# Kernel optimization log

Measured on AMD Instinct MI355X. Metric: run time of the kernel, lower is better.

Reference implementation:

```python
import jax, jax.numpy as jnp
import numpy as np

H = 2048   # hidden_size
NH = 16    # num_heads
D = 128    # head_dim_qk == head_dim_v
K = 4      # conv_kernel_size


def _causal_depthwise_conv(x, w, b):
    # x: [B,S,C], w: [C,K], b: [C]. Matches torch Conv1d(groups=C, padding=K-1)[..., :S]
    S = x.shape[1]
    xp = jnp.pad(x, ((0, 0), (K - 1, 0), (0, 0)))
    y = b
    for j in range(K):
        y = y + xp[:, j:j + S, :] * w[:, j]
    return y


def setup_inputs() -> dict:
    key = jax.random.key(0)
    ks = jax.random.split(key, 18)
    s = 0.02
    B, S = 2, 2048
    return {
        "x": jax.random.normal(ks[0], (B, S, H), dtype=jnp.float32),
        "Wq": jax.random.normal(ks[1], (H, NH * D), dtype=jnp.float32) * s,
        "Wk": jax.random.normal(ks[2], (H, NH * D), dtype=jnp.float32) * s,
        "Wv": jax.random.normal(ks[3], (H, NH * D), dtype=jnp.float32) * s,
        "Wa": jax.random.normal(ks[4], (H, NH), dtype=jnp.float32) * s,
        "ba": jax.random.normal(ks[5], (NH,), dtype=jnp.float32) * s,
        "Wb": jax.random.normal(ks[6], (H, NH), dtype=jnp.float32) * s,
        "bb": jax.random.normal(ks[7], (NH,), dtype=jnp.float32) * s,
        "Wg": jax.random.normal(ks[8], (H, NH * D), dtype=jnp.float32) * s,
        "Wo": jax.random.normal(ks[9], (NH * D, H), dtype=jnp.float32) * s,
        "qcw": jax.random.normal(ks[10], (NH * D, K), dtype=jnp.float32) * s,
        "qcb": jax.random.normal(ks[11], (NH * D,), dtype=jnp.float32) * s,
        "kcw": jax.random.normal(ks[12], (NH * D, K), dtype=jnp.float32) * s,
        "kcb": jax.random.normal(ks[13], (NH * D,), dtype=jnp.float32) * s,
        "vcw": jax.random.normal(ks[14], (NH * D, K), dtype=jnp.float32) * s,
        "vcb": jax.random.normal(ks[15], (NH * D,), dtype=jnp.float32) * s,
        "ln_w": jnp.ones((D,), dtype=jnp.float32),
        "ln_b": jnp.zeros((D,), dtype=jnp.float32),
    }


def _forward(x, Wq, Wk, Wv, Wa, ba, Wb, bb, Wg, Wo,
             qcw, qcb, kcw, kcb, vcw, vcb, ln_w, ln_b):
    B, S, _ = x.shape
    q = _causal_depthwise_conv(x @ Wq, qcw, qcb)
    k = _causal_depthwise_conv(x @ Wk, kcw, kcb)
    v = _causal_depthwise_conv(x @ Wv, vcw, vcb)
    q = jax.nn.silu(q).reshape(B, S, NH, D)
    k = jax.nn.silu(k).reshape(B, S, NH, D) * (D ** -0.5)
    v = jax.nn.silu(v).reshape(B, S, NH, D)
    alpha = jax.nn.sigmoid(x @ Wa + ba)  # [B,S,NH]
    beta = jax.nn.sigmoid(x @ Wb + bb)   # [B,S,NH]

    # time-major for scan
    qt = jnp.moveaxis(q, 1, 0)       # [S,B,NH,D]
    kt = jnp.moveaxis(k, 1, 0)
    vt = jnp.moveaxis(v, 1, 0)
    at = jnp.moveaxis(alpha, 1, 0)   # [S,B,NH]
    bt = jnp.moveaxis(beta, 1, 0)

    def step(St, inp):
        q_, k_, v_, a_, b_ = inp
        sk = jnp.einsum('bhij,bhj->bhi', St, k_)            # [B,NH,D]
        err = sk - v_
        Sn = (a_[..., None, None] * St
              - b_[..., None, None] * err[..., None] * k_[..., None, :])
        o_ = jnp.einsum('bhij,bhj->bhi', Sn, q_)
        return Sn, o_

    S0 = jnp.zeros((B, NH, D, D), dtype=x.dtype)
    _, o = jax.lax.scan(step, S0, (qt, kt, vt, at, bt))
    o = jnp.moveaxis(o, 0, 1)  # [B,S,NH,D]

    # LayerNorm over head_dim
    mu = jnp.mean(o, axis=-1, keepdims=True)
    var = jnp.mean(jnp.square(o - mu), axis=-1, keepdims=True)
    o = (o - mu) * jax.lax.rsqrt(var + 1e-5) * ln_w + ln_b

    g = jax.nn.sigmoid(x @ Wg).reshape(B, S, NH, D)
    o = (o * g).reshape(B, S, NH * D)
    return o @ Wo


def reference(x, Wq, Wk, Wv, Wa, ba, Wb, bb, Wg, Wo,
              qcw, qcb, kcw, kcb, vcw, vcb, ln_w, ln_b):
    return _forward(x, Wq, Wk, Wv, Wa, ba, Wb, bb, Wg, Wo,
                    qcw, qcb, kcw, kcb, vcw, vcb, ln_w, ln_b)
```

## Files before the change

kernel.cpp:

```cpp
#include <hip/hip_runtime.h>
#include <math.h>
#include <stdint.h>

typedef unsigned short u16;
typedef unsigned int u32;
typedef __attribute__((ext_vector_type(8))) short short8;
typedef __attribute__((ext_vector_type(4))) float f32x4;

#define MFMA16(a, b, c) __builtin_amdgcn_mfma_f32_16x16x32_bf16(a, b, c, 0, 0, 0)

__device__ __forceinline__ u16 f2bf(float f) {
  union { float f; u32 u; } v; v.f = f;
  return (u16)((v.u + 0x7FFFu + ((v.u >> 16) & 1u)) >> 16);
}
__device__ __forceinline__ float bf2f(u16 h) {
  union { u32 u; float f; } v; v.u = ((u32)h) << 16; return v.f;
}
__device__ __forceinline__ float bflo(u32 p) {
  union { u32 u; float f; } v; v.u = p << 16; return v.f;
}
__device__ __forceinline__ float bfhi(u32 p) {
  union { u32 u; float f; } v; v.u = p & 0xffff0000u; return v.f;
}
__device__ __forceinline__ float sigm(float x) { return 1.f / (1.f + expf(-x)); }

__global__ void k_cvt_x(const float* __restrict__ x, u16* __restrict__ xb) {
  int i = (blockIdx.x * 256 + threadIdx.x) * 8;
  float4 a = *(const float4*)(x + i);
  float4 b = *(const float4*)(x + i + 4);
  uint4 p;
  p.x = (u32)f2bf(a.x) | ((u32)f2bf(a.y) << 16);
  p.y = (u32)f2bf(a.z) | ((u32)f2bf(a.w) << 16);
  p.z = (u32)f2bf(b.x) | ((u32)f2bf(b.y) << 16);
  p.w = (u32)f2bf(b.z) | ((u32)f2bf(b.w) << 16);
  *(uint4*)(xb + i) = p;
}

__global__ void k_tconv4(const float* __restrict__ W0, const float* __restrict__ W1,
                         const float* __restrict__ W2, const float* __restrict__ W3,
                         u16* __restrict__ Wt) {
  __shared__ float tile[32][33];
  int z = blockIdx.z;
  const float* W = (z == 0) ? W0 : (z == 1) ? W1 : (z == 2) ? W2 : W3;
  u16* dst = Wt + (size_t)z * 2048 * 2048;
  int n0 = blockIdx.x * 32, k0 = blockIdx.y * 32;
  int tc = threadIdx.x & 31, tr = threadIdx.x >> 5;
  #pragma unroll
  for (int p = 0; p < 4; ++p) {
    int k = k0 + p * 8 + tr;
    tile[p * 8 + tr][tc] = W[(size_t)k * 2048 + n0 + tc];
  }
  __syncthreads();
  #pragma unroll
  for (int p = 0; p < 4; ++p) {
    int n = n0 + p * 8 + tr;
    dst[(size_t)n * 2048 + k0 + tc] = f2bf(tile[tc][p * 8 + tr]);
  }
}

__global__ void k_tconv(const float* __restrict__ W, u16* __restrict__ Wt) {
  __shared__ float tile[32][33];
  int n0 = blockIdx.x * 32, k0 = blockIdx.y * 32;
  int tc = threadIdx.x & 31, tr = threadIdx.x >> 5;
  #pragma unroll
  for (int p = 0; p < 4; ++p) {
    int k = k0 + p * 8 + tr;
    tile[p * 8 + tr][tc] = W[(size_t)k * 2048 + n0 + tc];
  }
  __syncthreads();
  #pragma unroll
  for (int p = 0; p < 4; ++p) {
    int n = n0 + p * 8 + tr;
    Wt[(size_t)n * 2048 + k0 + tc] = f2bf(tile[tc][p * 8 + tr]);
  }
}

__global__ __launch_bounds__(256)
void k_ab(const float* __restrict__ x, const float* __restrict__ Wa,
          const float* __restrict__ ba, const float* __restrict__ Wb,
          const float* __restrict__ bb, float* __restrict__ ab2) {
  __shared__ float Wl[128 * 32];
  __shared__ float xl[8][128];
  const int t = threadIdx.x;
  const int lr = t >> 5, c = t & 31;
  const int r0 = blockIdx.x * 8;
  const int ch = c & 15;
  float acc = 0.f;
  for (int kt = 0; kt < 16; ++kt) {
    #pragma unroll
    for (int i = 0; i < 16; ++i) {
      int idx = i * 256 + t;
      int kk = idx >> 5, cc = idx & 31;
      const float* Ws = (cc < 16) ? Wa : Wb;
      Wl[kk * 32 + cc] = Ws[(kt * 128 + kk) * 16 + (cc & 15)];
    }
    #pragma unroll
    for (int i = 0; i < 4; ++i) {
      int idx = i * 256 + t;
      int rr = idx >> 7, kk = idx & 127;
      xl[rr][kk] = x[(size_t)(r0 + rr) * 2048 + kt * 128 + kk];
    }
    __syncthreads();
    #pragma unroll
    for (int kk = 0; kk < 128; kk += 4) {
      float2 x01 = *(const float2*)&xl[lr][kk];
      float2 x23 = *(const float2*)&xl[lr][kk + 2];
      acc += x01.x * Wl[(kk + 0) * 32 + c] + x01.y * Wl[(kk + 1) * 32 + c]
           + x23.x * Wl[(kk + 2) * 32 + c] + x23.y * Wl[(kk + 3) * 32 + c];
    }
    __syncthreads();
  }
  acc += (c < 16) ? ba[ch] : bb[ch];
  float sg = sigm(acc);
  int rowi = r0 + lr;
  int b = rowi >> 11, s = rowi & 2047;
  size_t base = ((size_t)(b * 16 + ch) * 2048 + s) * 2;
  if (c < 16) ab2[base + 0] = sg;
  else        ab2[base + 1] = sg;
}

__device__ __forceinline__ void gld_lds16(const u16* g, u16* l) {
  __builtin_amdgcn_global_load_lds((const __attribute__((address_space(1))) void*)g,
                                   (__attribute__((address_space(3))) void*)l, 16, 0, 0);
}

template <int MODE>
__global__ void k_gemm(const u16* __restrict__ A, const u16* __restrict__ Bw,
                       void* C0, void* C1, int Kd) {
  __shared__ u16 As[2][128 * 32];
  __shared__ u16 Bs[2][128 * 32];
  const int t = threadIdx.x;
  const int lane = t & 63, wv = t >> 6;
  const int wr = wv >> 1, wc = wv & 1;
  const int m0 = blockIdx.y * 128, n0 = blockIdx.x * 128;
  f32x4 acc[4][4] = {};
  const int NT = Kd / 32;

  auto stage = [&](int buf, int kt) {
    #pragma unroll
    for (int i = 0; i < 2; ++i) {
      int li = i * 256 + t;
      int row = li >> 2, kc = li & 3;
      int kcs = kc ^ ((row >> 1) & 3);
      const u16* ga = A + (size_t)(m0 + row) * Kd + kt * 32 + kcs * 8;
      gld_lds16(ga, &As[buf][(i * 256 + wv * 64) * 8]);
      const u16* gb = Bw + (size_t)(n0 + row) * Kd + kt * 32 + kcs * 8;
      gld_lds16(gb, &Bs[buf][(i * 256 + wv * 64) * 8]);
    }
  };

  stage(0, 0);
  __syncthreads();
  int buf = 0;
  const int l15 = lane & 15, l4 = lane >> 4;
  for (int kt = 0; kt < NT; ++kt) {
    if (kt + 1 < NT) stage(buf ^ 1, kt + 1);
    short8 af[4], bfr[4];
    #pragma unroll
    for (int m = 0; m < 4; ++m) {
      int row = wr * 64 + m * 16 + l15;
      int g = l4 ^ ((row >> 1) & 3);
      af[m] = *(const short8*)&As[buf][row * 32 + g * 8];
    }
    #pragma unroll
    for (int n = 0; n < 4; ++n) {
      int row = wc * 64 + n * 16 + l15;
      int g = l4 ^ ((row >> 1) & 3);
      bfr[n] = *(const short8*)&Bs[buf][row * 32 + g * 8];
    }
    #pragma unroll
    for (int m = 0; m < 4; ++m)
      #pragma unroll
      for (int n = 0; n < 4; ++n)
        acc[m][n] = MFMA16(af[m], bfr[n], acc[m][n]);
    __syncthreads();
    buf ^= 1;
  }
  #pragma unroll
  for (int m = 0; m < 4; ++m)
    #pragma unroll
    for (int n = 0; n < 4; ++n)
      #pragma unroll
      for (int e = 0; e < 4; ++e) {
        int row = m0 + wr * 64 + m * 16 + l4 * 4 + e;
        int col = n0 + wc * 64 + n * 16 + l15;
        if (MODE == 0) {
          ((float*)C0)[(size_t)row * 2048 + col] = acc[m][n][e];
        } else {
          u16 vb = f2bf(acc[m][n][e]);
          if (n0 < 6144) ((u16*)C0)[(size_t)row * 6144 + col] = vb;
          else           ((u16*)C1)[(size_t)row * 2048 + (col - 6144)] = vb;
        }
      }
}

template <int MODE>
__global__ __launch_bounds__(512)
void k_gemm8(const u16* __restrict__ A, const u16* __restrict__ Bw,
             void* C0, void* C1) {
  __shared__ u16 lds[65536];
  const int t = threadIdx.x;
  const int w = t >> 6, lane = t & 63;
  const int l15 = lane & 15, l4 = lane >> 4;
  const int wm = w >> 2, wn = w & 3;
  const int bid = blockIdx.x;
  const int mt = ((bid & 7) << 1) | ((bid >> 3) & 1);
  const int nt = bid >> 4;
  const int m0 = mt * 256, n0 = nt * 256;

  f32x4 acc[8][4] = {};
  short8 a[4][2], b[4][2];

  auto stageHalf = [&](int buf, int kt, int mat, int half) {
    const u16* src = mat ? Bw : A;
    const int row0 = (mat ? n0 : m0) + half * 128;
    u16* dst0 = &lds[mat * 32768 + (buf * 2 + half) * 8192 + w * 1024];
    #pragma unroll
    for (int i = 0; i < 2; ++i) {
      int f = w * 128 + i * 64 + lane;
      int rr = f >> 3, g = f & 7;
      const u16* ga = src + (size_t)(row0 + rr) * 2048 + kt * 64 + ((g ^ (rr & 7)) << 3);
      gld_lds16(ga, dst0 + i * 512);
    }
  };
  auto rdA = [&](int buf, int mq, int ks) {
    int row = wm * 64 + (mq & 3) * 16 + l15;
    int g = (l4 + ks * 4) ^ (row & 7);
    return *(const short8*)&lds[(buf * 2 + (mq >> 2)) * 8192 + row * 64 + g * 8];
  };
  auto rdB = [&](int buf, int n, int ks) {
    int row = wn * 32 + (n & 1) * 16 + l15;
    int g = (l4 + ks * 4) ^ (row & 7);
    return *(const short8*)&lds[32768 + (buf * 2 + (n >> 1)) * 8192 + row * 64 + g * 8];
  };

  stageHalf(0, 0, 0, 0); stageHalf(0, 0, 1, 0);
  stageHalf(0, 0, 1, 1); stageHalf(0, 0, 0, 1);
  asm volatile("s_waitcnt vmcnt(0)" ::: "memory");
  __builtin_amdgcn_s_barrier();
  __builtin_amdgcn_sched_barrier(0);

  for (int kt = 0; kt < 32; ++kt) {
    const int bufc = kt & 1, bufn = bufc ^ 1;
    const int ktn = (kt + 1 < 32) ? kt + 1 : 31;

    stageHalf(bufn, ktn, 0, 0);
    stageHalf(bufn, ktn, 1, 0);
    stageHalf(bufn, ktn, 1, 1);
    #pragma unroll
    for (int mq = 0; mq < 4; ++mq) { a[mq][0] = rdA(bufc, mq, 0); a[mq][1] = rdA(bufc, mq, 1); }
    #pragma unroll
    for (int n = 0; n < 4; ++n) { b[n][0] = rdB(bufc, n, 0); b[n][1] = rdB(bufc, n, 1); }
    __builtin_amdgcn_s_setprio(1);
    #pragma unroll
    for (int mq = 0; mq < 4; ++mq)
      #pragma unroll
      for (int n = 0; n < 4; ++n) {
        acc[mq][n] = MFMA16(a[mq][0], b[n][0], acc[mq][n]);
        acc[mq][n] = MFMA16(a[mq][1], b[n][1], acc[mq][n]);
      }
    __builtin_amdgcn_s_setprio(0);
    asm volatile("s_waitcnt vmcnt(6)" ::: "memory");
    __builtin_amdgcn_s_barrier();
    __builtin_amdgcn_sched_barrier(0);

    stageHalf(bufn, ktn, 0, 1);
    #pragma unroll
    for (int mq = 0; mq < 4; ++mq) { a[mq][0] = rdA(bufc, mq + 4, 0); a[mq][1] = rdA(bufc, mq + 4, 1); }
    __builtin_amdgcn_s_setprio(1);
    #pragma unroll
    for (int mq = 0; mq < 4; ++mq)
      #pragma unroll
      for (int n = 0; n < 4; ++n) {
        acc[mq + 4][n] = MFMA16(a[mq][0], b[n][0], acc[mq + 4][n]);
        acc[mq + 4][n] = MFMA16(a[mq][1], b[n][1], acc[mq + 4][n]);
      }
    __builtin_amdgcn_s_setprio(0);
    asm volatile("s_waitcnt vmcnt(2)" ::: "memory");
    __builtin_amdgcn_s_barrier();
    __builtin_amdgcn_sched_barrier(0);
  }

  const bool toG = (MODE == 1) && (n0 >= 6144);
  #pragma unroll
  for (int mq = 0; mq < 8; ++mq) {
    int row = m0 + (mq >> 2) * 128 + wm * 64 + (mq & 3) * 16 + l4 * 4;
    #pragma unroll
    for (int n = 0; n < 4; ++n) {
      int col = n0 + (n >> 1) * 128 + wn * 32 + (n & 1) * 16 + l15;
      #pragma unroll
      for (int e = 0; e < 4; ++e) {
        if (MODE == 0) {
          ((float*)C0)[(size_t)(row + e) * 2048 + col] = acc[mq][n][e];
        } else {
          u16 vb = f2bf(acc[mq][n][e]);
          if (!toG) ((u16*)C0)[(size_t)(row + e) * 6144 + col] = vb;
          else      ((u16*)C1)[(size_t)(row + e) * 2048 + (col - 6144)] = vb;
        }
      }
    }
  }
}

__global__ void k_conv(const u16* __restrict__ projQKV,
                       const float* __restrict__ qcw, const float* __restrict__ qcb,
                       const float* __restrict__ kcw, const float* __restrict__ kcb,
                       const float* __restrict__ vcw, const float* __restrict__ vcb,
                       u16* __restrict__ qkv2) {
  int idx = blockIdx.x * 256 + threadIdx.x;
  int cq = idx % 1536, rrow = idx / 1536;
  int c = cq * 4;
  int s = rrow & 2047, b = rrow >> 11;
  int type = c >> 11;
  int ch = c & 2047;
  int h = ch >> 7, d = ch & 127;
  const float* cw; const float* cb;
  if (type == 0)      { cw = qcw; cb = qcb; }
  else if (type == 1) { cw = kcw; cb = kcb; }
  else                { cw = vcw; cb = vcb; }
  float wch[4][4];
  #pragma unroll
  for (int u = 0; u < 4; ++u) {
    float4 wv = *(const float4*)(cw + (ch + u) * 4);
    wch[u][0] = wv.x; wch[u][1] = wv.y; wch[u][2] = wv.z; wch[u][3] = wv.w;
  }
  float4 bv = *(const float4*)(cb + ch);
  float accv[4] = {bv.x, bv.y, bv.z, bv.w};
  #pragma unroll
  for (int j = 0; j < 4; ++j) {
    int sj = s - 3 + j;
    if (sj < 0) continue;
    const u16* p = projQKV + (size_t)(rrow + j - 3) * 6144 + c;
    u32 pa = *(const u32*)p;
    u32 pb = *(const u32*)(p + 2);
    accv[0] += bflo(pa) * wch[0][j];
    accv[1] += bfhi(pa) * wch[1][j];
    accv[2] += bflo(pb) * wch[2][j];
    accv[3] += bfhi(pb) * wch[3][j];
  }
  u16 o4[4];
  #pragma unroll
  for (int u = 0; u < 4; ++u) {
    float y = accv[u];
    float sv = y * sigm(y);
    if (type == 1) sv *= 0.08838834764831845f;
    o4[u] = f2bf(sv);
  }
  int off = (type == 1 ? 0 : (type == 0 ? 128 : 256)) + d;
  u16* dst = qkv2 + ((size_t)(b * 16 + h) * 2048 + s) * 384 + off;
  *(u32*)dst       = (u32)o4[0] | ((u32)o4[1] << 16);
  *(u32*)(dst + 2) = (u32)o4[2] | ((u32)o4[3] << 16);
}

__global__ __launch_bounds__(256)
void k_chunkA(const u16* __restrict__ qkv2, const float* __restrict__ ab2,
              u16* __restrict__ Tbv, u16* __restrict__ nTbk,
              u16* __restrict__ Aq, float* __restrict__ vecs,
              u16* __restrict__ Kt) {
  __shared__ u16 Kl[64][136], Ql[64][136];
  __shared__ float Gk[4096], Gq[4096];
  __shared__ float clL[64], laL[64], bL[64], gpL[64];
  const int unit = blockIdx.x;
  const int bh = unit >> 5, c = unit & 31;
  const int t = threadIdx.x;
  const int wv = t >> 6, lane = t & 63;
  const int l15 = lane & 15, l4 = lane >> 4;
  const u16* qb = qkv2 + ((size_t)bh * 2048 + c * 64) * 384;

  #pragma unroll
  for (int p = 0; p < 4; ++p) {
    int ld = p * 256 + t;
    int row = ld >> 4, c8 = (ld & 15) * 8;
    *(uint4*)&Kl[row][c8] = *(const uint4*)(qb + (size_t)row * 384 + c8);
    *(uint4*)&Ql[row][c8] = *(const uint4*)(qb + (size_t)row * 384 + 128 + c8);
  }
  if (wv == 0) {
    float2 abv = *(const float2*)(ab2 + ((size_t)bh * 2048 + c * 64 + lane) * 2);
    float la = log2f(abv.x);
    float cl = la;
    #pragma unroll
    for (int o = 1; o < 64; o <<= 1) {
      float nv = __shfl_up(cl, o, 64);
      if (lane >= o) cl += nv;
    }
    clL[lane] = cl; laL[lane] = la; bL[lane] = abv.y;
    gpL[lane] = exp2f(cl - la);
  }
  __syncthreads();

  {
    const int t0 = (wv >> 1) * 32, i0 = (wv & 1) * 32;
    f32x4 ak[2][2] = {}, aq[2][2] = {};
    #pragma unroll
    for (int ks = 0; ks < 4; ++ks) {
      short8 bk[2], Ka[2], Qa[2];
      #pragma unroll
      for (int n = 0; n < 2; ++n)
        bk[n] = *(const short8*)&Kl[i0 + n * 16 + l15][ks * 32 + l4 * 8];
      #pragma unroll
      for (int m = 0; m < 2; ++m) {
        Ka[m] = *(const short8*)&Kl[t0 + m * 16 + l15][ks * 32 + l4 * 8];
        Qa[m] = *(const short8*)&Ql[t0 + m * 16 + l15][ks * 32 + l4 * 8];
      }
      #pragma unroll
      for (int m = 0; m < 2; ++m)
        #pragma unroll
        for (int n = 0; n < 2; ++n) {
          ak[m][n] = MFMA16(Ka[m], bk[n], ak[m][n]);
          aq[m][n] = MFMA16(Qa[m], bk[n], aq[m][n]);
        }
    }
    #pragma unroll
    for (int m = 0; m < 2; ++m)
      #pragma unroll
      for (int n = 0; n < 2; ++n)
        #pragma unroll
        for (int e = 0; e < 4; ++e) {
          int row = t0 + m * 16 + l4 * 4 + e;
          int col = i0 + n * 16 + l15;
          Gk[row * 64 + col] = ak[m][n][e];
          Gq[row * 64 + col] = aq[m][n][e];
        }
  }
  __syncthreads();

  #pragma unroll
  for (int p = 0; p < 16; ++p) {
    int e = p * 256 + t; int tt = e >> 6, ii = e & 63;
    float lv = 0.f;
    if (ii < tt) lv = bL[tt] * Gk[e] * exp2f(clL[tt] - laL[tt] - clL[ii]);
    float av = (ii <= tt) ? Gq[e] * exp2f(clL[tt] - clL[ii]) : 0.f;
    Gk[e] = lv;
    Aq[(size_t)unit * 4096 + e] = f2bf(av);
  }
  __syncthreads();

  float X[64];
  if (t < 128) {
    #pragma unroll
    for (int r = 0; r < 64; ++r)
      X[r] = bL[r] * bf2f(qb[(size_t)r * 384 + 256 + t]);
  } else {
    int ck = t - 128;
    #pragma unroll
    for (int r = 0; r < 64; ++r)
      X[r] = -bL[r] * gpL[r] * bf2f(Kl[r][ck]);
  }
  #pragma unroll
  for (int i = 0; i < 63; ++i) {
    float xi = X[i];
    #pragma unroll
    for (int r = i + 1; r < 64; ++r)
      X[r] = fmaf(-Gk[r * 64 + i], xi, X[r]);
  }
  if (t < 128) {
    #pragma unroll
    for (int r = 0; r < 64; ++r)
      Tbv[(size_t)unit * 8192 + r * 128 + t] = f2bf(X[r]);
  } else {
    #pragma unroll
    for (int r = 0; r < 64; ++r)
      nTbk[(size_t)unit * 8192 + r * 128 + (t - 128)] = f2bf(X[r]);
  }
  if (t < 64) {
    vecs[(size_t)unit * 128 + t] = exp2f(clL[t]);
    vecs[(size_t)unit * 128 + 64 + t] = exp2f(clL[63] - clL[t]);
  }
  {
    int dk = t >> 1, tt0 = (t & 1) * 32;
    uint4 w[4];
    u16* wp = (u16*)w;
    #pragma unroll
    for (int j = 0; j < 32; ++j) wp[j] = Kl[tt0 + j][dk];
    uint4* dst = (uint4*)(Kt + (size_t)unit * 8192 + dk * 64 + tt0);
    dst[0] = w[0]; dst[1] = w[1]; dst[2] = w[2]; dst[3] = w[3];
  }
}

#define OFF_NT  0
#define OFF_AQ  8192
#define OFF_Q   12288
#define OFF_KT  20480
#define OFF_TBV 28672
#define STG_U16 29696

__global__ __launch_bounds__(256)
void k_chunkB(const u16* __restrict__ qkv2, const u16* __restrict__ Tbv,
              const u16* __restrict__ nTbk, const u16* __restrict__ Aq,
              const u16* __restrict__ Kt, const float* __restrict__ vecs,
              float* __restrict__ o) {
  __shared__ u16 stg[2][STG_U16];
  __shared__ float S[16 * 132];
  __shared__ u16 Ut[16 * 72], Utd[16 * 72];
  __shared__ float gdl[2][128];
  const int bid = blockIdx.x;
  const int xcd = bid & 7, within = bid >> 3;
  const int sl = within & 7, hgrp = within >> 3;
  const int bh = hgrp * 8 + xcd;
  const int dv0 = sl * 16;
  const int b = bh >> 4, h = bh & 15;
  const int t = threadIdx.x;
  const int wv = t >> 6, lane = t & 63;
  const int l15 = lane & 15, l4 = lane >> 4;
  const int t0 = wv * 16;
  const int dk0 = wv * 32;
  const u16* qbase = qkv2 + (size_t)bh * 2048 * 384;
  float* obase = o + (size_t)b * 2048 * 2048 + h * 128 + dv0;

  for (int p = t; p < 16 * 132; p += 256) S[p] = 0.f;

  auto stage = [&](int buf, int c) {
    u16* sb = &stg[buf][0];
    const size_t unit = (size_t)bh * 32 + c;
    const u16* tbk = nTbk + unit * 8192;
    const u16* aqp = Aq + unit * 4096;
    const u16* ktp = Kt + unit * 8192;
    const u16* tbv = Tbv + unit * 8192;
    const u16* qp  = qbase + (size_t)c * 64 * 384 + 128;
    #pragma unroll
    for (int r = 0; r < 4; ++r) {
      int f = r * 256 + t; int rr = f >> 4, c16 = f & 15;
      gld_lds16(tbk + rr * 128 + (c16 ^ (rr & 7)) * 8, sb + OFF_NT + (r * 256 + wv * 64) * 8);
    }
    #pragma unroll
    for (int r = 0; r < 2; ++r) {
      int f = r * 256 + t; int rr = f >> 3, c8 = f & 7;
      gld_lds16(aqp + rr * 64 + (c8 ^ (rr & 7)) * 8, sb + OFF_AQ + (r * 256 + wv * 64) * 8);
    }
    #pragma unroll
    for (int r = 0; r < 4; ++r) {
      int f = r * 256 + t; int rr = f >> 4, c16 = f & 15;
      gld_lds16(qp + rr * 384 + (c16 ^ (rr & 7)) * 8, sb + OFF_Q + (r * 256 + wv * 64) * 8);
    }
    #pragma unroll
    for (int r = 0; r < 4; ++r) {
      int f = r * 256 + t; int rr = f >> 3, c8 = f & 7;
      gld_lds16(ktp + rr * 64 + (c8 ^ (rr & 7)) * 8, sb + OFF_KT + (r * 256 + wv * 64) * 8);
    }
    if (t < 128)
      gld_lds16(tbv + (t >> 1) * 128 + dv0 + (t & 1) * 8, sb + OFF_TBV + wv * 64 * 8);
  };

  stage(0, 0);
  if (t < 128) gdl[0][t] = vecs[(size_t)bh * 32 * 128 + t];
  __syncthreads();

  for (int c = 0; c < 32; ++c) {
    const int buf = c & 1;
    const u16* sb = &stg[buf][0];
    float vnext = 0.f;
    if (c + 1 < 32) {
      stage(buf ^ 1, c + 1);
      if (t < 128) vnext = vecs[((size_t)bh * 32 + c + 1) * 128 + t];
    }

    f32x4 acc1 = {}, acc2 = {};
    #pragma unroll
    for (int e = 0; e < 4; ++e)
      acc1[e] = bf2f(sb[OFF_TBV + (t0 + l4 * 4 + e) * 16 + l15]);
    #pragma unroll
    for (int ks = 0; ks < 4; ++ks) {
      short8 bhi, blo;
      {
        const float* srow = &S[l15 * 132 + ks * 32 + l4 * 8];
        float4 s0 = *(const float4*)srow, s1 = *(const float4*)(srow + 4);
        float sv[8] = {s0.x, s0.y, s0.z, s0.w, s1.x, s1.y, s1.z, s1.w};
        #pragma unroll
        for (int j = 0; j < 8; ++j) {
          u16 hv = f2bf(sv[j]);
          bhi[j] = (short)hv;
          blo[j] = (short)f2bf(sv[j] - bf2f(hv));
        }
      }
      const int cx = ((ks * 4 + l4) ^ (l15 & 7)) * 8;
      short8 a1 = *(const short8*)&sb[OFF_NT + (t0 + l15) * 128 + cx];
      short8 a2 = *(const short8*)&sb[OFF_Q + (t0 + l15) * 128 + cx];
      acc1 = MFMA16(a1, bhi, acc1);
      acc1 = MFMA16(a1, blo, acc1);
      acc2 = MFMA16(a2, bhi, acc2);
      acc2 = MFMA16(a2, blo, acc2);
    }
    {
      u16 up[4], ud[4];
      #pragma unroll
      for (int e = 0; e < 4; ++e) {
        float uv = acc1[e];
        up[e] = f2bf(uv);
        ud[e] = f2bf(uv * gdl[buf][64 + t0 + l4 * 4 + e]);
      }
      int ux = l15 * 72 + t0 + l4 * 4;
      *(u32*)&Ut[ux]      = (u32)up[0] | ((u32)up[1] << 16);
      *(u32*)&Ut[ux + 2]  = (u32)up[2] | ((u32)up[3] << 16);
      *(u32*)&Utd[ux]     = (u32)ud[0] | ((u32)ud[1] << 16);
      *(u32*)&Utd[ux + 2] = (u32)ud[2] | ((u32)ud[3] << 16);
    }
    asm volatile("s_waitcnt lgkmcnt(0)" ::: "memory");
    __builtin_amdgcn_s_barrier();
    __builtin_amdgcn_sched_barrier(0);

    #pragma unroll
    for (int e = 0; e < 4; ++e) acc2[e] *= gdl[buf][t0 + l4 * 4 + e];
    #pragma unroll
    for (int ks = 0; ks < 2; ++ks) {
      const int cx = ((ks * 4 + l4) ^ (l15 & 7)) * 8;
      short8 af = *(const short8*)&sb[OFF_AQ + (t0 + l15) * 64 + cx];
      short8 bf_ = *(const short8*)&Ut[l15 * 72 + ks * 32 + l4 * 8];
      acc2 = MFMA16(af, bf_, acc2);
    }
    #pragma unroll
    for (int e = 0; e < 4; ++e)
      obase[(size_t)(c * 64 + t0 + l4 * 4 + e) * 2048 + l15] = acc2[e];

    f32x4 acc3[2] = {};
    #pragma unroll
    for (int ks = 0; ks < 2; ++ks) {
      short8 a3 = *(const short8*)&Utd[l15 * 72 + ks * 32 + l4 * 8];
      #pragma unroll
      for (int n = 0; n < 2; ++n) {
        const int kr = dk0 + n * 16 + l15;
        const int cx = ((ks * 4 + l4) ^ (l15 & 7)) * 8;
        short8 b3 = *(const short8*)&sb[OFF_KT + kr * 64 + cx];
        acc3[n] = MFMA16(a3, b3, acc3[n]);
      }
    }
    float gtot = gdl[buf][63];
    #pragma unroll
    for (int n = 0; n < 2; ++n)
      #pragma unroll
      for (int e = 0; e < 4; ++e) {
        float* sp = &S[(l4 * 4 + e) * 132 + dk0 + n * 16 + l15];
        *sp = gtot * *sp + acc3[n][e];
      }
    if (c + 1 < 32 && t < 128) gdl[buf ^ 1][t] = vnext;
    __syncthreads();
  }
}

__global__ void k_lng(const float* __restrict__ o, const u16* __restrict__ projG,
                      const float* __restrict__ ln_w, const float* __restrict__ ln_b,
                      u16* __restrict__ og) {
  int gidx = blockIdx.x * 4 + (threadIdx.x >> 6);
  int lane = threadIdx.x & 63;
  int rrow = gidx >> 4, h = gidx & 15;
  const float* op = o + (size_t)rrow * 2048 + h * 128;
  float2 x2 = *(const float2*)(op + lane * 2);
  float sum = x2.x + x2.y, sq = x2.x * x2.x + x2.y * x2.y;
  #pragma unroll
  for (int m = 1; m < 64; m <<= 1) {
    sum += __shfl_xor(sum, m, 64);
    sq  += __shfl_xor(sq, m, 64);
  }
  float mu = sum * (1.f / 128.f);
  float var = sq * (1.f / 128.f) - mu * mu;
  float rs = 1.0f / sqrtf(var + 1e-5f);
  u32 gu = *(const u32*)(projG + (size_t)rrow * 2048 + h * 128 + lane * 2);
  float g0 = sigm(bflo(gu)), g1 = sigm(bfhi(gu));
  int d0 = lane * 2;
  float y0 = ((x2.x - mu) * rs * ln_w[d0] + ln_b[d0]) * g0;
  float y1 = ((x2.y - mu) * rs * ln_w[d0 + 1] + ln_b[d0 + 1]) * g1;
  *(u32*)(og + (size_t)rrow * 2048 + h * 128 + d0) = (u32)f2bf(y0) | ((u32)f2bf(y1) << 16);
}

extern "C" void kernel_launch(void* const* d_in, const int* in_sizes, int n_in,
                              void* d_out, int out_size, void* d_ws, size_t ws_size,
                              hipStream_t stream) {
  const float* x   = (const float*)d_in[0];
  const float* Wq  = (const float*)d_in[1];
  const float* Wk  = (const float*)d_in[2];
  const float* Wv  = (const float*)d_in[3];
  const float* Wa  = (const float*)d_in[4];
  const float* ba  = (const float*)d_in[5];
  const float* Wb  = (const float*)d_in[6];
  const float* bb  = (const float*)d_in[7];
  const float* Wg  = (const float*)d_in[8];
  const float* Wo  = (const float*)d_in[9];
  const float* qcw = (const float*)d_in[10];
  const float* qcb = (const float*)d_in[11];
  const float* kcw = (const float*)d_in[12];
  const float* kcb = (const float*)d_in[13];
  const float* vcw = (const float*)d_in[14];
  const float* vcb = (const float*)d_in[15];
  const float* lnw = (const float*)d_in[16];
  const float* lnb = (const float*)d_in[17];
  float* out = (float*)d_out;

  if (ws_size < 168820736ull) return;
  char* ws = (char*)d_ws;
  u16*   xb   = (u16*)(ws);
  u16*   Kt   = (u16*)(ws);
  u16*   og   = (u16*)(ws);
  u16*   Wt   = (u16*)(ws + 16777216);
  u16*   Wot  = (u16*)(ws + 16777216);
  u16*   Tbv  = (u16*)(ws + 25165824);
  u16*   Aq   = (u16*)(ws + 41943040);
  u16*   pQKV = (u16*)(ws + 50331648);
  float* oB   = (float*)(ws + 50331648);
  u16*   nTbk = (u16*)(ws + 83886080);
  u16*   pG   = (u16*)(ws + 100663296);
  u16*   qkv2 = (u16*)(ws + 117440512);
  float* ab2  = (float*)(ws + 167772160);
  float* vecs = (float*)(ws + 168296448);

  k_cvt_x<<<4096, 256, 0, stream>>>(x, xb);
  k_tconv4<<<dim3(64, 64, 4), 256, 0, stream>>>(Wq, Wk, Wv, Wg, Wt);
  k_ab<<<512, 256, 0, stream>>>(x, Wa, ba, Wb, bb, ab2);

  k_gemm8<1><<<512, 512, 0, stream>>>(xb, Wt, pQKV, pG);
  k_tconv<<<dim3(64, 64), 256, 0, stream>>>(Wo, Wot);
  k_conv<<<24576, 256, 0, stream>>>(pQKV, qcw, qcb, kcw, kcb, vcw, vcb, qkv2);
  k_chunkA<<<1024, 256, 0, stream>>>(qkv2, ab2, Tbv, nTbk, Aq, vecs, Kt);
  k_chunkB<<<256, 256, 0, stream>>>(qkv2, Tbv, nTbk, Aq, Kt, vecs, oB);
  k_lng<<<16384, 256, 0, stream>>>(oB, pG, lnw, lnb, og);
  k_gemm<0><<<dim3(16, 32), 256, 0, stream>>>(og, Wot, out, nullptr, 2048);
}
```

Before: 465.5 us.

## Restructure QKVG GEMM main loop into 8-phase ping-pong schedule with quarter-tile staging

Rewrites the k_gemm8 main loop to process two k-tiles per iteration in eight phases. Each phase interleaves LDS fragment reads, one half-tile global-to-LDS stage, and a quarter of the MFMA block, separated by barriers, with both buffers preloaded before the loop. The aim is finer overlap of global loads, LDS reads and matrix math across waves. The block mapping also changes from a swizzled 1D grid to a plain 2D grid, which gives up the L2-friendly tile ordering and adds many more barriers per k-tile.

```diff
diff --git a/kernel.cpp b/kernel.cpp
--- a/kernel.cpp
+++ b/kernel.cpp
@@ -194,6 +194,10 @@
       }
 }
 
+#define SBAR __builtin_amdgcn_s_barrier()
+#define SCHB __builtin_amdgcn_sched_barrier(0)
+#define LGKM0 asm volatile("s_waitcnt lgkmcnt(0)" ::: "memory")
+
 template <int MODE>
 __global__ __launch_bounds__(512)
 void k_gemm8(const u16* __restrict__ A, const u16* __restrict__ Bw,
@@ -203,10 +207,7 @@
   const int w = t >> 6, lane = t & 63;
   const int l15 = lane & 15, l4 = lane >> 4;
   const int wm = w >> 2, wn = w & 3;
-  const int bid = blockIdx.x;
-  const int mt = ((bid & 7) << 1) | ((bid >> 3) & 1);
-  const int nt = bid >> 4;
-  const int m0 = mt * 256, n0 = nt * 256;
+  const int m0 = blockIdx.y * 256, n0 = blockIdx.x * 256;
 
   f32x4 acc[8][4] = {};
   short8 a[4][2], b[4][2];
@@ -233,52 +234,83 @@
     int g = (l4 + ks * 4) ^ (row & 7);
     return *(const short8*)&lds[32768 + (buf * 2 + (n >> 1)) * 8192 + row * 64 + g * 8];
   };
-
-  stageHalf(0, 0, 0, 0); stageHalf(0, 0, 1, 0);
-  stageHalf(0, 0, 1, 1); stageHalf(0, 0, 0, 1);
+  auto quad = [&](int mB, int nB) {
+    #pragma unroll
+    for (int mq = 0; mq < 4; ++mq)
+      #pragma unroll
+      for (int nn = 0; nn < 2; ++nn) {
+        acc[mB + mq][nB + nn] = MFMA16(a[mq][0], b[nB + nn][0], acc[mB + mq][nB + nn]);
+        acc[mB + mq][nB + nn] = MFMA16(a[mq][1], b[nB + nn][1], acc[mB + mq][nB + nn]);
+      }
+  };
+
+  stageHalf(0, 0, 0, 0); stageHalf(0, 0, 1, 0); stageHalf(0, 0, 1, 1); stageHalf(0, 0, 0, 1);
+  stageHalf(1, 1, 0, 0); stageHalf(1, 1, 1, 0); stageHalf(1, 1, 1, 1); stageHalf(1, 1, 0, 1);
   asm volatile("s_waitcnt vmcnt(0)" ::: "memory");
-  __builtin_amdgcn_s_barrier();
-  __builtin_amdgcn_sched_barrier(0);
-
-  for (int kt = 0; kt < 32; ++kt) {
-    const int bufc = kt & 1, bufn = bufc ^ 1;
-    const int ktn = (kt + 1 < 32) ? kt + 1 : 31;
-
-    stageHalf(bufn, ktn, 0, 0);
-    stageHalf(bufn, ktn, 1, 0);
-    stageHalf(bufn, ktn, 1, 1);
-    #pragma unroll
-    for (int mq = 0; mq < 4; ++mq) { a[mq][0] = rdA(bufc, mq, 0); a[mq][1] = rdA(bufc, mq, 1); }
-    #pragma unroll
-    for (int n = 0; n < 4; ++n) { b[n][0] = rdB(bufc, n, 0); b[n][1] = rdB(bufc, n, 1); }
-    __builtin_amdgcn_s_setprio(1);
-    #pragma unroll
-    for (int mq = 0; mq < 4; ++mq)
-      #pragma unroll
-      for (int n = 0; n < 4; ++n) {
-        acc[mq][n] = MFMA16(a[mq][0], b[n][0], acc[mq][n]);
-        acc[mq][n] = MFMA16(a[mq][1], b[n][1], acc[mq][n]);
-      }
-    __builtin_amdgcn_s_setprio(0);
+  SBAR; SCHB;
+
+  for (int it = 0; it < 16; ++it) {
+    const int kt0 = 2 * it;
+    const int st0 = (it < 15) ? kt0 + 2 : kt0;
+    const int st1 = (it < 15) ? kt0 + 3 : kt0 + 1;
+
+    #pragma unroll
+    for (int mq = 0; mq < 4; ++mq) { a[mq][0] = rdA(0, mq, 0); a[mq][1] = rdA(0, mq, 1); }
+    #pragma unroll
+    for (int n = 0; n < 2; ++n) { b[n][0] = rdB(0, n, 0); b[n][1] = rdB(0, n, 1); }
+    SCHB; SBAR; LGKM0; SCHB;
+    __builtin_amdgcn_s_setprio(1); quad(0, 0); __builtin_amdgcn_s_setprio(0);
+    SBAR; SCHB;
+
+    #pragma unroll
+    for (int n = 2; n < 4; ++n) { b[n][0] = rdB(0, n, 0); b[n][1] = rdB(0, n, 1); }
+    stageHalf(0, st0, 0, 0);
+    SCHB; SBAR; LGKM0; SCHB;
+    __builtin_amdgcn_s_setprio(1); quad(0, 2); __builtin_amdgcn_s_setprio(0);
+    SBAR; SCHB;
+
+    #pragma unroll
+    for (int mq = 0; mq < 4; ++mq) { a[mq][0] = rdA(0, mq + 4, 0); a[mq][1] = rdA(0, mq + 4, 1); }
+    stageHalf(0, st0, 1, 0);
+    SCHB; SBAR; LGKM0; SCHB;
+    __builtin_amdgcn_s_setprio(1); quad(4, 2); __builtin_amdgcn_s_setprio(0);
+    SBAR; SCHB;
+
+    stageHalf(0, st0, 1, 1);
+    SCHB; SBAR; LGKM0; SCHB;
+    __builtin_amdgcn_s_setprio(1); quad(4, 0); __builtin_amdgcn_s_setprio(0);
     asm volatile("s_waitcnt vmcnt(6)" ::: "memory");
-    __builtin_amdgcn_s_barrier();
-    __builtin_amdgcn_sched_barrier(0);
-
-    stageHalf(bufn, ktn, 0, 1);
-    #pragma unroll
-    for (int mq = 0; mq < 4; ++mq) { a[mq][0] = rdA(bufc, mq + 4, 0); a[mq][1] = rdA(bufc, mq + 4, 1); }
-    __builtin_amdgcn_s_setprio(1);
-    #pragma unroll
-    for (int mq = 0; mq < 4; ++mq)
-      #pragma unroll
-      for (int n = 0; n < 4; ++n) {
-        acc[mq + 4][n] = MFMA16(a[mq][0], b[n][0], acc[mq + 4][n]);
-        acc[mq + 4][n] = MFMA16(a[mq][1], b[n][1], acc[mq + 4][n]);
-      }
-    __builtin_amdgcn_s_setprio(0);
-    asm volatile("s_waitcnt vmcnt(2)" ::: "memory");
-    __builtin_amdgcn_s_barrier();
-    __builtin_amdgcn_sched_barrier(0);
+    SBAR; SCHB;
+
+    #pragma unroll
+    for (int mq = 0; mq < 4; ++mq) { a[mq][0] = rdA(1, mq, 0); a[mq][1] = rdA(1, mq, 1); }
+    #pragma unroll
+    for (int n = 0; n < 2; ++n) { b[n][0] = rdB(1, n, 0); b[n][1] = rdB(1, n, 1); }
+    stageHalf(0, st0, 0, 1);
+    SCHB; SBAR; LGKM0; SCHB;
+    __builtin_amdgcn_s_setprio(1); quad(0, 0); __builtin_amdgcn_s_setprio(0);
+    SBAR; SCHB;
+
+    #pragma unroll
+    for (int n = 2; n < 4; ++n) { b[n][0] = rdB(1, n, 0); b[n][1] = rdB(1, n, 1); }
+    stageHalf(1, st1, 0, 0);
+    SCHB; SBAR; LGKM0; SCHB;
+    __builtin_amdgcn_s_setprio(1); quad(0, 2); __builtin_amdgcn_s_setprio(0);
+    SBAR; SCHB;
+
+    #pragma unroll
+    for (int mq = 0; mq < 4; ++mq) { a[mq][0] = rdA(1, mq + 4, 0); a[mq][1] = rdA(1, mq + 4, 1); }
+    stageHalf(1, st1, 1, 0);
+    SCHB; SBAR; LGKM0; SCHB;
+    __builtin_amdgcn_s_setprio(1); quad(4, 2); __builtin_amdgcn_s_setprio(0);
+    SBAR; SCHB;
+
+    stageHalf(1, st1, 1, 1);
+    stageHalf(1, st1, 0, 1);
+    SCHB; SBAR; LGKM0; SCHB;
+    __builtin_amdgcn_s_setprio(1); quad(4, 0); __builtin_amdgcn_s_setprio(0);
+    asm volatile("s_waitcnt vmcnt(8)" ::: "memory");
+    SBAR; SCHB;
   }
 
   const bool toG = (MODE == 1) && (n0 >= 6144);
@@ -705,7 +737,7 @@
   k_tconv4<<<dim3(64, 64, 4), 256, 0, stream>>>(Wq, Wk, Wv, Wg, Wt);
   k_ab<<<512, 256, 0, stream>>>(x, Wa, ba, Wb, bb, ab2);
 
-  k_gemm8<1><<<512, 512, 0, stream>>>(xb, Wt, pQKV, pG);
+  k_gemm8<1><<<dim3(32, 16), 512, 0, stream>>>(xb, Wt, pQKV, pG);
   k_tconv<<<dim3(64, 64), 256, 0, stream>>>(Wo, Wot);
   k_conv<<<24576, 256, 0, stream>>>(pQKV, qcw, qcb, kcw, kcb, vcw, vcb, qkv2);
   k_chunkA<<<1024, 256, 0, stream>>>(qkv2, ab2, Tbv, nTbk, Aq, vecs, Kt);
```

Measured after the change: 471.7 us. About the same (+1.3%).

## Simplify QKVG GEMM to single-phase K=32 double-buffered loop with plain syncs

Applied to the files above, without the earlier changes.

Replaces the hand-scheduled two-phase K=64 pipeline in the fused QKV/gate GEMM with a simpler loop over K=32 tiles, halving LDS usage. It drops the staggered half-tile staging, vmcnt waits, priority hints and the swizzled block-to-tile mapping, switching to a 2D grid and __syncthreads. Less LDS may allow more occupancy, but it doubles barrier count and loses fine-grained overlap and L2-friendly tile ordering.

```diff
diff --git a/kernel.cpp b/kernel.cpp
--- a/kernel.cpp
+++ b/kernel.cpp
@@ -198,87 +198,55 @@
 __global__ __launch_bounds__(512)
 void k_gemm8(const u16* __restrict__ A, const u16* __restrict__ Bw,
              void* C0, void* C1) {
-  __shared__ u16 lds[65536];
+  __shared__ u16 lds[32768];
   const int t = threadIdx.x;
   const int w = t >> 6, lane = t & 63;
   const int l15 = lane & 15, l4 = lane >> 4;
   const int wm = w >> 2, wn = w & 3;
-  const int bid = blockIdx.x;
-  const int mt = ((bid & 7) << 1) | ((bid >> 3) & 1);
-  const int nt = bid >> 4;
-  const int m0 = mt * 256, n0 = nt * 256;
+  const int m0 = blockIdx.y * 256, n0 = blockIdx.x * 256;
 
   f32x4 acc[8][4] = {};
-  short8 a[4][2], b[4][2];
-
-  auto stageHalf = [&](int buf, int kt, int mat, int half) {
-    const u16* src = mat ? Bw : A;
-    const int row0 = (mat ? n0 : m0) + half * 128;
-    u16* dst0 = &lds[mat * 32768 + (buf * 2 + half) * 8192 + w * 1024];
+
+  auto stage = [&](int buf, int kt) {
     #pragma unroll
     for (int i = 0; i < 2; ++i) {
       int f = w * 128 + i * 64 + lane;
-      int rr = f >> 3, g = f & 7;
-      const u16* ga = src + (size_t)(row0 + rr) * 2048 + kt * 64 + ((g ^ (rr & 7)) << 3);
-      gld_lds16(ga, dst0 + i * 512);
+      int rr = f >> 2, g = f & 3;
+      int gs = g ^ ((rr >> 1) & 3);
+      const u16* ga = A + (size_t)(m0 + rr) * 2048 + kt * 32 + gs * 8;
+      gld_lds16(ga, &lds[buf * 8192 + f * 8]);
+      const u16* gb = Bw + (size_t)(n0 + rr) * 2048 + kt * 32 + gs * 8;
+      gld_lds16(gb, &lds[16384 + buf * 8192 + f * 8]);
     }
   };
-  auto rdA = [&](int buf, int mq, int ks) {
-    int row = wm * 64 + (mq & 3) * 16 + l15;
-    int g = (l4 + ks * 4) ^ (row & 7);
-    return *(const short8*)&lds[(buf * 2 + (mq >> 2)) * 8192 + row * 64 + g * 8];
+  auto rdA = [&](int buf, int mq) {
+    int row = (mq >> 2) * 128 + wm * 64 + (mq & 3) * 16 + l15;
+    int g = l4 ^ ((row >> 1) & 3);
+    return *(const short8*)&lds[buf * 8192 + row * 32 + g * 8];
   };
-  auto rdB = [&](int buf, int n, int ks) {
-    int row = wn * 32 + (n & 1) * 16 + l15;
-    int g = (l4 + ks * 4) ^ (row & 7);
-    return *(const short8*)&lds[32768 + (buf * 2 + (n >> 1)) * 8192 + row * 64 + g * 8];
+  auto rdB = [&](int buf, int n) {
+    int row = (n >> 1) * 128 + wn * 32 + (n & 1) * 16 + l15;
+    int g = l4 ^ ((row >> 1) & 3);
+    return *(const short8*)&lds[16384 + buf * 8192 + row * 32 + g * 8];
   };
 
-  stageHalf(0, 0, 0, 0); stageHalf(0, 0, 1, 0);
-  stageHalf(0, 0, 1, 1); stageHalf(0, 0, 0, 1);
-  asm volatile("s_waitcnt vmcnt(0)" ::: "memory");
-  __builtin_amdgcn_s_barrier();
-  __builtin_amdgcn_sched_barrier(0);
-
-  for (int kt = 0; kt < 32; ++kt) {
-    const int bufc = kt & 1, bufn = bufc ^ 1;
-    const int ktn = (kt + 1 < 32) ? kt + 1 : 31;
-
-    stageHalf(bufn, ktn, 0, 0);
-    stageHalf(bufn, ktn, 1, 0);
-    stageHalf(bufn, ktn, 1, 1);
-    #pragma unroll
-    for (int mq = 0; mq < 4; ++mq) { a[mq][0] = rdA(bufc, mq, 0); a[mq][1] = rdA(bufc, mq, 1); }
-    #pragma unroll
-    for (int n = 0; n < 4; ++n) { b[n][0] = rdB(bufc, n, 0); b[n][1] = rdB(bufc, n, 1); }
-    __builtin_amdgcn_s_setprio(1);
-    #pragma unroll
-    for (int mq = 0; mq < 4; ++mq)
-      #pragma unroll
-      for (int n = 0; n < 4; ++n) {
-        acc[mq][n] = MFMA16(a[mq][0], b[n][0], acc[mq][n]);
-        acc[mq][n] = MFMA16(a[mq][1], b[n][1], acc[mq][n]);
-      }
-    __builtin_amdgcn_s_setprio(0);
-    asm volatile("s_waitcnt vmcnt(6)" ::: "memory");
-    __builtin_amdgcn_s_barrier();
-    __builtin_amdgcn_sched_barrier(0);
-
-    stageHalf(bufn, ktn, 0, 1);
-    #pragma unroll
-    for (int mq = 0; mq < 4; ++mq) { a[mq][0] = rdA(bufc, mq + 4, 0); a[mq][1] = rdA(bufc, mq + 4, 1); }
-    __builtin_amdgcn_s_setprio(1);
-    #pragma unroll
-    for (int mq = 0; mq < 4; ++mq)
-      #pragma unroll
-      for (int n = 0; n < 4; ++n) {
-        acc[mq + 4][n] = MFMA16(a[mq][0], b[n][0], acc[mq + 4][n]);
-        acc[mq + 4][n] = MFMA16(a[mq][1], b[n][1], acc[mq + 4][n]);
-      }
-    __builtin_amdgcn_s_setprio(0);
-    asm volatile("s_waitcnt vmcnt(2)" ::: "memory");
-    __builtin_amdgcn_s_barrier();
-    __builtin_amdgcn_sched_barrier(0);
+  stage(0, 0);
+  __syncthreads();
+
+  for (int kt = 0; kt < 64; ++kt) {
+    const int buf = kt & 1;
+    if (kt + 1 < 64) stage(buf ^ 1, kt + 1);
+    short8 a[8], b[4];
+    #pragma unroll
+    for (int mq = 0; mq < 8; ++mq) a[mq] = rdA(buf, mq);
+    #pragma unroll
+    for (int n = 0; n < 4; ++n) b[n] = rdB(buf, n);
+    #pragma unroll
+    for (int mq = 0; mq < 8; ++mq)
+      #pragma unroll
+      for (int n = 0; n < 4; ++n)
+        acc[mq][n] = MFMA16(a[mq], b[n], acc[mq][n]);
+    __syncthreads();
   }
 
   const bool toG = (MODE == 1) && (n0 >= 6144);
@@ -705,7 +673,7 @@
   k_tconv4<<<dim3(64, 64, 4), 256, 0, stream>>>(Wq, Wk, Wv, Wg, Wt);
   k_ab<<<512, 256, 0, stream>>>(x, Wa, ba, Wb, bb, ab2);
 
-  k_gemm8<1><<<512, 512, 0, stream>>>(xb, Wt, pQKV, pG);
+  k_gemm8<1><<<dim3(32, 16), 512, 0, stream>>>(xb, Wt, pQKV, pG);
   k_tconv<<<dim3(64, 64), 256, 0, stream>>>(Wo, Wot);
   k_conv<<<24576, 256, 0, stream>>>(pQKV, qcw, qcb, kcw, kcb, vcw, vcb, qkv2);
   k_chunkA<<<1024, 256, 0, stream>>>(qkv2, ab2, Tbv, nTbk, Aq, vecs, Kt);
```

New measurement: 470.9 us. No clear change (+1.2%).

## Fuse causal conv and SiLU into chunkA, drop separate conv kernel

Applied to the files above, without the earlier changes.

Removes the standalone k_conv kernel and its qkv2 intermediate buffer. chunkA now computes the depthwise causal conv and SiLU for q, k and v directly from the projection output, and writes a compact Q buffer for chunkB. The gemm8 grid is also changed from a swizzled 1D block mapping to a plain 2D grid. This saves a full write and read of the qkv2 intermediate, at the cost of redundant halo row loads and more work inside chunkA. The gemm8 grid change may lose the cache locality the swizzle was providing.

```diff
diff --git a/kernel.cpp b/kernel.cpp
--- a/kernel.cpp
+++ b/kernel.cpp
@@ -203,10 +203,7 @@
   const int w = t >> 6, lane = t & 63;
   const int l15 = lane & 15, l4 = lane >> 4;
   const int wm = w >> 2, wn = w & 3;
-  const int bid = blockIdx.x;
-  const int mt = ((bid & 7) << 1) | ((bid >> 3) & 1);
-  const int nt = bid >> 4;
-  const int m0 = mt * 256, n0 = nt * 256;
+  const int m0 = blockIdx.y * 256, n0 = blockIdx.x * 256;
 
   f32x4 acc[8][4] = {};
   short8 a[4][2], b[4][2];
@@ -302,77 +299,79 @@
   }
 }
 
-__global__ void k_conv(const u16* __restrict__ projQKV,
-                       const float* __restrict__ qcw, const float* __restrict__ qcb,
-                       const float* __restrict__ kcw, const float* __restrict__ kcb,
-                       const float* __restrict__ vcw, const float* __restrict__ vcb,
-                       u16* __restrict__ qkv2) {
-  int idx = blockIdx.x * 256 + threadIdx.x;
-  int cq = idx % 1536, rrow = idx / 1536;
-  int c = cq * 4;
-  int s = rrow & 2047, b = rrow >> 11;
-  int type = c >> 11;
-  int ch = c & 2047;
-  int h = ch >> 7, d = ch & 127;
-  const float* cw; const float* cb;
-  if (type == 0)      { cw = qcw; cb = qcb; }
-  else if (type == 1) { cw = kcw; cb = kcb; }
-  else                { cw = vcw; cb = vcb; }
-  float wch[4][4];
-  #pragma unroll
-  for (int u = 0; u < 4; ++u) {
-    float4 wv = *(const float4*)(cw + (ch + u) * 4);
-    wch[u][0] = wv.x; wch[u][1] = wv.y; wch[u][2] = wv.z; wch[u][3] = wv.w;
-  }
-  float4 bv = *(const float4*)(cb + ch);
-  float accv[4] = {bv.x, bv.y, bv.z, bv.w};
-  #pragma unroll
-  for (int j = 0; j < 4; ++j) {
-    int sj = s - 3 + j;
-    if (sj < 0) continue;
-    const u16* p = projQKV + (size_t)(rrow + j - 3) * 6144 + c;
-    u32 pa = *(const u32*)p;
-    u32 pb = *(const u32*)(p + 2);
-    accv[0] += bflo(pa) * wch[0][j];
-    accv[1] += bfhi(pa) * wch[1][j];
-    accv[2] += bflo(pb) * wch[2][j];
-    accv[3] += bfhi(pb) * wch[3][j];
-  }
-  u16 o4[4];
-  #pragma unroll
-  for (int u = 0; u < 4; ++u) {
-    float y = accv[u];
-    float sv = y * sigm(y);
-    if (type == 1) sv *= 0.08838834764831845f;
-    o4[u] = f2bf(sv);
-  }
-  int off = (type == 1 ? 0 : (type == 0 ? 128 : 256)) + d;
-  u16* dst = qkv2 + ((size_t)(b * 16 + h) * 2048 + s) * 384 + off;
-  *(u32*)dst       = (u32)o4[0] | ((u32)o4[1] << 16);
-  *(u32*)(dst + 2) = (u32)o4[2] | ((u32)o4[3] << 16);
-}
-
 __global__ __launch_bounds__(256)
-void k_chunkA(const u16* __restrict__ qkv2, const float* __restrict__ ab2,
+void k_chunkA(const u16* __restrict__ proj, const float* __restrict__ ab2,
+              const float* __restrict__ qcw, const float* __restrict__ qcb,
+              const float* __restrict__ kcw, const float* __restrict__ kcb,
+              const float* __restrict__ vcw, const float* __restrict__ vcb,
               u16* __restrict__ Tbv, u16* __restrict__ nTbk,
               u16* __restrict__ Aq, float* __restrict__ vecs,
-              u16* __restrict__ Kt) {
+              u16* __restrict__ Kt, u16* __restrict__ Qd) {
   __shared__ u16 Kl[64][136], Ql[64][136];
   __shared__ float Gk[4096], Gq[4096];
   __shared__ float clL[64], laL[64], bL[64], gpL[64];
   const int unit = blockIdx.x;
   const int bh = unit >> 5, c = unit & 31;
+  const int b = bh >> 4, h = bh & 15;
+  const int s0 = c * 64;
   const int t = threadIdx.x;
   const int wv = t >> 6, lane = t & 63;
   const int l15 = lane & 15, l4 = lane >> 4;
-  const u16* qb = qkv2 + ((size_t)bh * 2048 + c * 64) * 384;
-
-  #pragma unroll
-  for (int p = 0; p < 4; ++p) {
-    int ld = p * 256 + t;
-    int row = ld >> 4, c8 = (ld & 15) * 8;
-    *(uint4*)&Kl[row][c8] = *(const uint4*)(qb + (size_t)row * 384 + c8);
-    *(uint4*)&Ql[row][c8] = *(const uint4*)(qb + (size_t)row * 384 + 128 + c8);
+  const u16* projb = proj + (size_t)b * 2048 * 6144;
+
+  {
+    const int tr = t >> 4, c8 = (t & 15) * 8;
+    const int ch0 = h * 128 + c8;
+    float4 wk[8], wq[8];
+    float bk[8], bq[8];
+    #pragma unroll
+    for (int u = 0; u < 8; ++u) {
+      wk[u] = *(const float4*)(kcw + (ch0 + u) * 4);
+      wq[u] = *(const float4*)(qcw + (ch0 + u) * 4);
+    }
+    {
+      float4 b0 = *(const float4*)(kcb + ch0); float4 b1 = *(const float4*)(kcb + ch0 + 4);
+      bk[0]=b0.x; bk[1]=b0.y; bk[2]=b0.z; bk[3]=b0.w; bk[4]=b1.x; bk[5]=b1.y; bk[6]=b1.z; bk[7]=b1.w;
+      float4 c0 = *(const float4*)(qcb + ch0); float4 c1 = *(const float4*)(qcb + ch0 + 4);
+      bq[0]=c0.x; bq[1]=c0.y; bq[2]=c0.z; bq[3]=c0.w; bq[4]=c1.x; bq[5]=c1.y; bq[6]=c1.z; bq[7]=c1.w;
+    }
+    #pragma unroll
+    for (int p = 0; p < 4; ++p) {
+      int row = p * 16 + tr;
+      int s = s0 + row;
+      float ak[8], aq_[8];
+      #pragma unroll
+      for (int u = 0; u < 8; ++u) { ak[u] = bk[u]; aq_[u] = bq[u]; }
+      #pragma unroll
+      for (int j = 0; j < 4; ++j) {
+        int sj = s - 3 + j;
+        if (sj < 0) continue;
+        const u16* rk = projb + (size_t)sj * 6144 + 2048 + ch0;
+        const u16* rq = projb + (size_t)sj * 6144 + ch0;
+        uint4 k4 = *(const uint4*)rk;
+        uint4 q4 = *(const uint4*)rq;
+        float kv[8] = {bflo(k4.x), bfhi(k4.x), bflo(k4.y), bfhi(k4.y),
+                       bflo(k4.z), bfhi(k4.z), bflo(k4.w), bfhi(k4.w)};
+        float qv[8] = {bflo(q4.x), bfhi(q4.x), bflo(q4.y), bfhi(q4.y),
+                       bflo(q4.z), bfhi(q4.z), bflo(q4.w), bfhi(q4.w)};
+        #pragma unroll
+        for (int u = 0; u < 8; ++u) {
+          float wkj = (j == 0) ? wk[u].x : (j == 1) ? wk[u].y : (j == 2) ? wk[u].z : wk[u].w;
+          float wqj = (j == 0) ? wq[u].x : (j == 1) ? wq[u].y : (j == 2) ? wq[u].z : wq[u].w;
+          ak[u] += kv[u] * wkj;
+          aq_[u] += qv[u] * wqj;
+        }
+      }
+      #pragma unroll
+      for (int u = 0; u < 8; ++u) {
+        float yk = ak[u];
+        float sk_ = yk * sigm(yk) * 0.08838834764831845f;
+        float yq = aq_[u];
+        float sq_ = yq * sigm(yq);
+        Kl[row][c8 + u] = f2bf(sk_);
+        Ql[row][c8 + u] = f2bf(sq_);
+      }
+    }
   }
   if (wv == 0) {
     float2 abv = *(const float2*)(ab2 + ((size_t)bh * 2048 + c * 64 + lane) * 2);
@@ -437,9 +436,24 @@
 
   float X[64];
   if (t < 128) {
-    #pragma unroll
-    for (int r = 0; r < 64; ++r)
-      X[r] = bL[r] * bf2f(qb[(size_t)r * 384 + 256 + t]);
+    const int chv = h * 128 + t;
+    float4 wv4 = *(const float4*)(vcw + chv * 4);
+    float vb = vcb[chv];
+    const u16* vcol = projb + 4096 + chv;
+    float wa = 0.f, wb_ = 0.f, wc_ = 0.f;
+    if (s0 > 0) {
+      wa = bf2f(vcol[(size_t)(s0 - 3) * 6144]);
+      wb_ = bf2f(vcol[(size_t)(s0 - 2) * 6144]);
+      wc_ = bf2f(vcol[(size_t)(s0 - 1) * 6144]);
+    }
+    #pragma unroll
+    for (int r = 0; r < 64; ++r) {
+      float wd = bf2f(vcol[(size_t)(s0 + r) * 6144]);
+      float y = vb + wa * wv4.x + wb_ * wv4.y + wc_ * wv4.z + wd * wv4.w;
+      float sv = y * sigm(y);
+      X[r] = bL[r] * bf2f(f2bf(sv));
+      wa = wb_; wb_ = wc_; wc_ = wd;
+    }
   } else {
     int ck = t - 128;
     #pragma unroll
@@ -474,6 +488,14 @@
     for (int j = 0; j < 32; ++j) wp[j] = Kl[tt0 + j][dk];
     uint4* dst = (uint4*)(Kt + (size_t)unit * 8192 + dk * 64 + tt0);
     dst[0] = w[0]; dst[1] = w[1]; dst[2] = w[2]; dst[3] = w[3];
+  }
+  {
+    const int tr = t >> 4, c8 = (t & 15) * 8;
+    #pragma unroll
+    for (int p = 0; p < 4; ++p) {
+      int row = p * 16 + tr;
+      *(uint4*)(Qd + (size_t)unit * 8192 + row * 128 + c8) = *(const uint4*)&Ql[row][c8];
+    }
   }
 }
 
@@ -485,7 +507,7 @@
 #define STG_U16 29696
 
 __global__ __launch_bounds__(256)
-void k_chunkB(const u16* __restrict__ qkv2, const u16* __restrict__ Tbv,
+void k_chunkB(const u16* __restrict__ Qd, const u16* __restrict__ Tbv,
               const u16* __restrict__ nTbk, const u16* __restrict__ Aq,
               const u16* __restrict__ Kt, const float* __restrict__ vecs,
               float* __restrict__ o) {
@@ -504,7 +526,6 @@
   const int l15 = lane & 15, l4 = lane >> 4;
   const int t0 = wv * 16;
   const int dk0 = wv * 32;
-  const u16* qbase = qkv2 + (size_t)bh * 2048 * 384;
   float* obase = o + (size_t)b * 2048 * 2048 + h * 128 + dv0;
 
   for (int p = t; p < 16 * 132; p += 256) S[p] = 0.f;
@@ -516,7 +537,7 @@
     const u16* aqp = Aq + unit * 4096;
     const u16* ktp = Kt + unit * 8192;
     const u16* tbv = Tbv + unit * 8192;
-    const u16* qp  = qbase + (size_t)c * 64 * 384 + 128;
+    const u16* qp  = Qd + unit * 8192;
     #pragma unroll
     for (int r = 0; r < 4; ++r) {
       int f = r * 256 + t; int rr = f >> 4, c16 = f & 15;
@@ -530,7 +551,7 @@
     #pragma unroll
     for (int r = 0; r < 4; ++r) {
       int f = r * 256 + t; int rr = f >> 4, c16 = f & 15;
-      gld_lds16(qp + rr * 384 + (c16 ^ (rr & 7)) * 8, sb + OFF_Q + (r * 256 + wv * 64) * 8);
+      gld_lds16(qp + rr * 128 + (c16 ^ (rr & 7)) * 8, sb + OFF_Q + (r * 256 + wv * 64) * 8);
     }
     #pragma unroll
     for (int r = 0; r < 4; ++r) {
@@ -695,9 +716,9 @@
   u16*   Aq   = (u16*)(ws + 41943040);
   u16*   pQKV = (u16*)(ws + 50331648);
   float* oB   = (float*)(ws + 50331648);
-  u16*   nTbk = (u16*)(ws + 83886080);
   u16*   pG   = (u16*)(ws + 100663296);
-  u16*   qkv2 = (u16*)(ws + 117440512);
+  u16*   Qd   = (u16*)(ws + 117440512);
+  u16*   nTbk = (u16*)(ws + 134217728);
   float* ab2  = (float*)(ws + 167772160);
   float* vecs = (float*)(ws + 168296448);
 
@@ -705,11 +726,11 @@
   k_tconv4<<<dim3(64, 64, 4), 256, 0, stream>>>(Wq, Wk, Wv, Wg, Wt);
   k_ab<<<512, 256, 0, stream>>>(x, Wa, ba, Wb, bb, ab2);
 
-  k_gemm8<1><<<512, 512, 0, stream>>>(xb, Wt, pQKV, pG);
+  k_gemm8<1><<<dim3(32, 16), 512, 0, stream>>>(xb, Wt, pQKV, pG);
   k_tconv<<<dim3(64, 64), 256, 0, stream>>>(Wo, Wot);
-  k_conv<<<24576, 256, 0, stream>>>(pQKV, qcw, qcb, kcw, kcb, vcw, vcb, qkv2);
-  k_chunkA<<<1024, 256, 0, stream>>>(qkv2, ab2, Tbv, nTbk, Aq, vecs, Kt);
-  k_chunkB<<<256, 256, 0, stream>>>(qkv2, Tbv, nTbk, Aq, Kt, vecs, oB);
+  k_chunkA<<<1024, 256, 0, stream>>>(pQKV, ab2, qcw, qcb, kcw, kcb, vcw, vcb,
+                                     Tbv, nTbk, Aq, vecs, Kt, Qd);
+  k_chunkB<<<256, 256, 0, stream>>>(Qd, Tbv, nTbk, Aq, Kt, vecs, oB);
   k_lng<<<16384, 256, 0, stream>>>(oB, pG, lnw, lnb, og);
   k_gemm<0><<<dim3(16, 32), 256, 0, stream>>>(og, Wot, out, nullptr, 2048);
 }
```

Result: faster. 451.5 us (-3.0%).
